# Performance work log

Hardware: AMD Instinct MI355X
Metric: run time of the kernel (lower is better)

The kernel has to match this reference:

```python
import jax, jax.numpy as jnp
import numpy as np
from jax import lax

B, C, L, G = 2048, 9605, 20, 50
ALPHA, ALPHA1, ALPHA2, ALPHA3, ALPHA_OTHER = 0.5, 0.05, 2.0, 10.0, 0.5
NEG_INF = jnp.float32(-1e30)


def setup_inputs() -> dict:
    k0, k1, k2, k3 = jax.random.split(jax.random.key(0), 4)
    x = jax.random.normal(k0, (B, C), jnp.float32)
    # sparse multi-label targets (~10 positives/row) so at most ~1 whitelist group is active,
    # matching the original code's assert len(gt_whitelist_index) == 1
    y = (jax.random.uniform(k1, (B, C)) < 0.001).astype(jnp.int32)
    y_neg = (jax.random.uniform(k2, (B, C)) < 0.001).astype(jnp.int32)
    # L disjoint whitelist groups of G classes each (from mapping_dict in the original)
    idx = jax.random.permutation(k3, C)[: L * G].reshape(L, G)
    group_mask = jnp.zeros((L, C), bool).at[jnp.arange(L)[:, None], idx].set(True)
    return {"x": x, "y": y, "y_neg": y_neg, "group_mask": group_mask}


def _rank_loss(x1, x2, margin):
    # our_rank_loss: sigmoid(alpha3*(x2-x1+margin)), scaled by alpha2 when positive
    d = x2 - x1 + margin
    s = jax.nn.sigmoid(ALPHA3 * d)
    return jnp.where(d > 0, ALPHA2 * s, s)


def reference(x, y, y_neg, group_mask):
    xs = jax.nn.sigmoid(x)  # [B, C]
    gmf = group_mask.astype(jnp.float32)  # [L, C]

    # per-row max score inside each whitelist group -> [B, L]
    # lax.map over the L (=20) groups keeps peak memory at one [B, C] temp per step
    group_max = lax.map(
        lambda m: jnp.max(jnp.where(m, xs, NEG_INF), axis=-1), group_mask
    ).T  # [B, L]

    # find_gt_whitelist: group k active iff sum(y[group_k]) > 0
    active = jnp.einsum("bc,lc->bl", y.astype(jnp.float32), gmf) > 0
    active_neg = jnp.einsum("bc,lc->bl", y_neg.astype(jnp.float32), gmf) > 0
    has_gt = jnp.any(active, axis=-1)  # [B]
    g = jnp.argmax(active, axis=-1)  # first active group (original asserts exactly one)

    # top_k_thres = max(11th largest sigmoid score, alpha_other) in both branches
    thres = jnp.maximum(lax.top_k(xs, 11)[0][:, 10], ALPHA_OTHER)  # [B]

    # max over union of all whitelist classes (wl_indices)
    union_max = jnp.max(jnp.where(jnp.any(group_mask, 0)[None, :], xs, NEG_INF), -1)

    gt_max = jnp.take_along_axis(group_max, g[:, None], axis=1)[:, 0]  # [B]
    # incorrect_max: max(0, max over groups != g); incorrect_neg: max(0, max over neg-active groups)
    excl = jnp.where(jnp.arange(L)[None, :] == g[:, None], NEG_INF, group_max)
    incorrect_max = jnp.maximum(jnp.max(excl, -1), 0.0)
    incorrect_neg = jnp.maximum(jnp.max(jnp.where(active_neg, group_max, 0.0), -1), 0.0)

    # branch A: no gt whitelist group active
    case_a = (1 - ALPHA) * _rank_loss(thres, union_max, ALPHA1) + ALPHA * _rank_loss(
        thres, incorrect_neg, ALPHA1
    )
    # branch B: exactly one gt group g
    case_b = (
        _rank_loss(gt_max, thres, ALPHA1)
        + jnp.where(
            incorrect_max > 0, (1 - ALPHA) * _rank_loss(thres, incorrect_max, ALPHA1), 0.0
        )
        + jnp.where(
            incorrect_neg > 0,
            ALPHA * _rank_loss(thres, incorrect_neg, ALPHA1),
            ALPHA * _rank_loss(thres, incorrect_max, ALPHA1),
        )
    )
    return jnp.sum(jnp.where(has_gt, case_b, case_a))
```

## Files before the change

### kernel.cpp

```cpp
#include <hip/hip_runtime.h>
#include <stdint.h>

#define B_ROWS 2048
#define C_CLS  9605
#define L_GRP  20
#define WAVES  4
#define UNROLL 8

__device__ __forceinline__ float sigmoidf(float v) {
  return 1.0f / (1.0f + __expf(-v));
}

__device__ __forceinline__ float rank_loss(float x1, float x2) {
  float d = x2 - x1 + 0.05f;
  float s = 1.0f / (1.0f + __expf(-10.0f * d));
  return d > 0.0f ? 2.0f * s : s;
}

__device__ __forceinline__ unsigned fmap(float f) {
  unsigned u = __float_as_uint(f);
  return (u & 0x80000000u) ? ~u : (u | 0x80000000u);
}
__device__ __forceinline__ float funmap(unsigned m) {
  unsigned u = (m & 0x80000000u) ? (m ^ 0x80000000u) : ~m;
  return __uint_as_float(u);
}

__global__ void probe_init_kernel(const unsigned char* __restrict__ gm,
                                  unsigned char* __restrict__ gid,
                                  int* __restrict__ cnt) {
  const int tid = blockIdx.x * blockDim.x + threadIdx.x;
  const int nthreads = gridDim.x * blockDim.x;
  for (int i = tid; i < C_CLS; i += nthreads) gid[i] = 0xFF;
  int local = 0;
  for (int i = tid; i < L_GRP * C_CLS; i += nthreads) local += (gm[i] != 0);
#pragma unroll
  for (int off = 32; off; off >>= 1) local += __shfl_xor(local, off);
  if ((threadIdx.x & 63) == 0 && local) atomicAdd(cnt, local);
}

__global__ void build_gid_kernel(const void* gm, const int* __restrict__ cnt,
                                 unsigned char* __restrict__ gid) {
  int i = blockIdx.x * blockDim.x + threadIdx.x;
  if (i >= L_GRP * C_CLS) return;
  const bool is_byte = (*cnt > 600);
  bool m;
  if (is_byte) m = ((const unsigned char*)gm)[i] != 0;
  else         m = ((const unsigned int*)gm)[i] != 0u;
  if (m) {
    int l = i / C_CLS;
    int c = i - l * C_CLS;
    gid[c] = (unsigned char)l;
  }
}

__global__ __launch_bounds__(WAVES * 64) void loss_kernel(
    const float* __restrict__ x, const int* __restrict__ y,
    const int* __restrict__ yn, const unsigned char* __restrict__ gid,
    float* __restrict__ out) {
  __shared__ unsigned s_gmax[WAVES][L_GRP];
  const int lane = threadIdx.x & 63;
  const int wave = threadIdx.x >> 6;
  const int row  = blockIdx.x * WAVES + wave;

  const float* xr = x  + (size_t)row * C_CLS;
  const int*   yr = y  + (size_t)row * C_CLS;
  const int*   nr = yn + (size_t)row * C_CLS;

  if (lane < L_GRP) s_gmax[wave][lane] = 0u;

  float t[11];
#pragma unroll
  for (int i = 0; i < 11; ++i) t[i] = -3.0e38f;
  unsigned actL = 0u, actnL = 0u;

  const int CM = (C_CLS / (64 * UNROLL)) * (64 * UNROLL);
  for (int c = lane; c < CM; c += 64 * UNROLL) {
    float xv[UNROLL]; int yv[UNROLL]; int nv[UNROLL]; unsigned char gv[UNROLL];
#pragma unroll
    for (int k = 0; k < UNROLL; ++k) {
      int cc = c + 64 * k;
      xv[k] = xr[cc]; yv[k] = yr[cc]; nv[k] = nr[cc]; gv[k] = gid[cc];
    }
#pragma unroll
    for (int k = 0; k < UNROLL; ++k) {
      float v = xv[k];
      if (v > t[10]) {
        float a = v;
#pragma unroll
        for (int i = 0; i < 11; ++i) { float hi = fmaxf(t[i], a); a = fminf(t[i], a); t[i] = hi; }
      }
      if (gv[k] < L_GRP) {
        atomicMax(&s_gmax[wave][gv[k]], fmap(v));
        unsigned bit = 1u << gv[k];
        if (yv[k] != 0) actL  |= bit;
        if (nv[k] != 0) actnL |= bit;
      }
    }
  }
  for (int c = CM + lane; c < C_CLS; c += 64) {
    float v = xr[c];
    unsigned char gk = gid[c];
    int yv = yr[c], nv = nr[c];
    if (v > t[10]) {
      float a = v;
#pragma unroll
      for (int i = 0; i < 11; ++i) { float hi = fmaxf(t[i], a); a = fminf(t[i], a); t[i] = hi; }
    }
    if (gk < L_GRP) {
      atomicMax(&s_gmax[wave][gk], fmap(v));
      unsigned bit = 1u << gk;
      if (yv != 0) actL  |= bit;
      if (nv != 0) actnL |= bit;
    }
  }

#pragma unroll
  for (int off = 32; off; off >>= 1) {
    actL  |= __shfl_xor(actL,  off);
    actnL |= __shfl_xor(actnL, off);
  }

  float cur = t[0];
  float eleventh = -3.0e38f;
#pragma unroll
  for (int r = 0; r < 11; ++r) {
    float m = cur;
#pragma unroll
    for (int off = 32; off; off >>= 1) m = fmaxf(m, __shfl_xor(m, off));
    eleventh = m;
    if (r < 10) {
      unsigned long long b = __ballot(cur == m);
      int leader = (int)(__ffsll(b) - 1);
      if (lane == leader) {
#pragma unroll
        for (int i = 0; i < 10; ++i) t[i] = t[i + 1];
        t[10] = -3.0e38f;
        cur = t[0];
      }
    }
  }

  __syncthreads();

  const bool has_gt = (actL != 0u);
  const int g = has_gt ? (__ffs(actL) - 1) : 0;
  const float thres = fmaxf(sigmoidf(eleventh), 0.5f);

  float union_max = -3.0e38f, gt_sg = 0.0f, inc_max = -3.0e38f, inc_neg = 0.0f;
#pragma unroll
  for (int l = 0; l < L_GRP; ++l) {
    float sg = sigmoidf(funmap(s_gmax[wave][l]));
    union_max = fmaxf(union_max, sg);
    if (l == g) gt_sg = sg; else inc_max = fmaxf(inc_max, sg);
    if ((actnL >> l) & 1u) inc_neg = fmaxf(inc_neg, sg);
  }
  inc_max = fmaxf(inc_max, 0.0f);
  inc_neg = fmaxf(inc_neg, 0.0f);

  float loss;
  if (has_gt) {
    loss = rank_loss(gt_sg, thres);
    if (inc_max > 0.0f) loss += 0.5f * rank_loss(thres, inc_max);
    loss += 0.5f * rank_loss(thres, (inc_neg > 0.0f) ? inc_neg : inc_max);
  } else {
    loss = 0.5f * rank_loss(thres, union_max) + 0.5f * rank_loss(thres, inc_neg);
  }
  if (lane == 0) atomicAdd(out, loss);
}

extern "C" void kernel_launch(void* const* d_in, const int* in_sizes, int n_in,
                              void* d_out, int out_size, void* d_ws, size_t ws_size,
                              hipStream_t stream) {
  (void)in_sizes; (void)n_in; (void)ws_size;
  const float* x  = (const float*)d_in[0];
  const int*   y  = (const int*)d_in[1];
  const int*   yn = (const int*)d_in[2];
  const void*  gm = d_in[3];

  int* cnt = (int*)d_ws;
  unsigned char* gid = (unsigned char*)d_ws + 64;

  hipMemsetAsync(d_ws, 0, 64, stream);
  probe_init_kernel<<<188, 256, 0, stream>>>((const unsigned char*)gm, gid, cnt);
  build_gid_kernel<<<(L_GRP * C_CLS + 255) / 256, 256, 0, stream>>>(gm, cnt, gid);

  hipMemsetAsync(d_out, 0, (size_t)out_size * sizeof(float), stream);

  loss_kernel<<<B_ROWS / WAVES, WAVES * 64, 0, stream>>>(x, y, yn, gid,
                                                         (float*)d_out);
}
```

Measured before the change: 264.7 us.

## Assign one block per row with vectorized aligned loads and replicated gid tables

The loss kernel now gives each row a full 256-thread block instead of one wave. Each row is read with float4/int4 loads after peeling to 16-byte alignment, and the gid table is stored as four shifted replicas so that each row's misalignment can use packed 4-byte gid reads. The per-wave top-11 results are merged through shared memory by wave 0, and the group state moves to shared atomics. The two memsets are folded into a single-block probe kernel, which trims launch overhead but serializes the gm scan on one block. The change also adds shared-memory atomics across the four waves and a __syncthreads.

Measured after the change: 252.8 us. -4.5%, faster.

```diff
diff --git a/kernel.cpp b/kernel.cpp
--- a/kernel.cpp
+++ b/kernel.cpp
@@ -4,8 +4,9 @@
 #define B_ROWS 2048
 #define C_CLS  9605
 #define L_GRP  20
-#define WAVES  4
-#define UNROLL 8
+#define GM_BYTES (L_GRP * C_CLS)
+#define REPSTRIDE 9728
+#define NEG_BIG -3.0e38f
 
 __device__ __forceinline__ float sigmoidf(float v) {
   return 1.0f / (1.0f + __expf(-v));
@@ -26,167 +27,214 @@
   return __uint_as_float(u);
 }
 
-__global__ void probe_init_kernel(const unsigned char* __restrict__ gm,
-                                  unsigned char* __restrict__ gid,
-                                  int* __restrict__ cnt) {
-  const int tid = blockIdx.x * blockDim.x + threadIdx.x;
-  const int nthreads = gridDim.x * blockDim.x;
-  for (int i = tid; i < C_CLS; i += nthreads) gid[i] = 0xFF;
+__global__ void probe_init_kernel(const uint4* __restrict__ gm,
+                                  unsigned char* __restrict__ ws,
+                                  float* __restrict__ out,
+                                  int* __restrict__ flag) {
+  __shared__ int s_part[16];
+  const int tid = threadIdx.x;
+  if (tid == 0) out[0] = 0.0f;
+  const int initbytes = 3 * REPSTRIDE + C_CLS + 16;
+  for (int i = tid; i < initbytes; i += 1024) ws[64 + i] = 0xFF;
   int local = 0;
-  for (int i = tid; i < L_GRP * C_CLS; i += nthreads) local += (gm[i] != 0);
+  const int nvec = GM_BYTES / 16;
+  for (int i = tid; i < nvec; i += 1024) {
+    uint4 w = gm[i];
+    unsigned a[4] = {w.x, w.y, w.z, w.w};
+#pragma unroll
+    for (int q = 0; q < 4; ++q) {
+      local += ((a[q] & 0x000000FFu) != 0) + ((a[q] & 0x0000FF00u) != 0) +
+               ((a[q] & 0x00FF0000u) != 0) + ((a[q] & 0xFF000000u) != 0);
+    }
+  }
+  if (tid == 0) {
+    const unsigned char* gb = (const unsigned char*)gm;
+    for (int i = nvec * 16; i < GM_BYTES; ++i) local += (gb[i] != 0);
+  }
 #pragma unroll
   for (int off = 32; off; off >>= 1) local += __shfl_xor(local, off);
-  if ((threadIdx.x & 63) == 0 && local) atomicAdd(cnt, local);
-}
-
-__global__ void build_gid_kernel(const void* gm, const int* __restrict__ cnt,
-                                 unsigned char* __restrict__ gid) {
+  if ((tid & 63) == 0) s_part[tid >> 6] = local;
+  __syncthreads();
+  if (tid == 0) {
+    int tot = 0;
+    for (int w = 0; w < 16; ++w) tot += s_part[w];
+    *flag = tot;
+  }
+}
+
+__global__ void build_gid_kernel(const void* gm, const int* __restrict__ flag,
+                                 unsigned char* __restrict__ ws) {
   int i = blockIdx.x * blockDim.x + threadIdx.x;
-  if (i >= L_GRP * C_CLS) return;
-  const bool is_byte = (*cnt > 600);
+  if (i >= GM_BYTES) return;
+  const bool is_byte = (*flag > 600);
   bool m;
   if (is_byte) m = ((const unsigned char*)gm)[i] != 0;
   else         m = ((const unsigned int*)gm)[i] != 0u;
   if (m) {
     int l = i / C_CLS;
     int c = i - l * C_CLS;
-    gid[c] = (unsigned char)l;
-  }
-}
-
-__global__ __launch_bounds__(WAVES * 64) void loss_kernel(
+    unsigned char* base = ws + 64;
+#pragma unroll
+    for (int r = 0; r < 4; ++r) base[r * REPSTRIDE + r + c] = (unsigned char)l;
+  }
+}
+
+__global__ __launch_bounds__(256, 4) void loss_kernel(
     const float* __restrict__ x, const int* __restrict__ y,
-    const int* __restrict__ yn, const unsigned char* __restrict__ gid,
+    const int* __restrict__ yn, const unsigned char* __restrict__ ws64,
     float* __restrict__ out) {
-  __shared__ unsigned s_gmax[WAVES][L_GRP];
-  const int lane = threadIdx.x & 63;
-  const int wave = threadIdx.x >> 6;
-  const int row  = blockIdx.x * WAVES + wave;
-
-  const float* xr = x  + (size_t)row * C_CLS;
-  const int*   yr = y  + (size_t)row * C_CLS;
-  const int*   nr = yn + (size_t)row * C_CLS;
-
-  if (lane < L_GRP) s_gmax[wave][lane] = 0u;
+  __shared__ unsigned s_gmax[L_GRP];
+  __shared__ unsigned s_act, s_actn;
+  __shared__ float s_wtop[4 * 11];
+  const int tid = threadIdx.x;
+  const int lane = tid & 63;
+  const int wave = tid >> 6;
+  const int row = blockIdx.x;
+
+  const size_t base = (size_t)row * C_CLS;
+  const int mis = (int)(base & 3);
+  const int peel = (4 - mis) & 3;
+  const float* xr = x + base;
+  const int* yr = y + base;
+  const int* nr = yn + base;
+  const unsigned char* gidc = ws64 + mis * REPSTRIDE + mis;
+
+  if (tid < L_GRP) s_gmax[tid] = 0u;
+  if (tid == 0) { s_act = 0u; s_actn = 0u; }
+  __syncthreads();
 
   float t[11];
 #pragma unroll
-  for (int i = 0; i < 11; ++i) t[i] = -3.0e38f;
+  for (int i = 0; i < 11; ++i) t[i] = NEG_BIG;
   unsigned actL = 0u, actnL = 0u;
 
-  const int CM = (C_CLS / (64 * UNROLL)) * (64 * UNROLL);
-  for (int c = lane; c < CM; c += 64 * UNROLL) {
-    float xv[UNROLL]; int yv[UNROLL]; int nv[UNROLL]; unsigned char gv[UNROLL];
-#pragma unroll
-    for (int k = 0; k < UNROLL; ++k) {
-      int cc = c + 64 * k;
-      xv[k] = xr[cc]; yv[k] = yr[cc]; nv[k] = nr[cc]; gv[k] = gid[cc];
-    }
-#pragma unroll
-    for (int k = 0; k < UNROLL; ++k) {
-      float v = xv[k];
-      if (v > t[10]) {
-        float a = v;
-#pragma unroll
-        for (int i = 0; i < 11; ++i) { float hi = fmaxf(t[i], a); a = fminf(t[i], a); t[i] = hi; }
-      }
-      if (gv[k] < L_GRP) {
-        atomicMax(&s_gmax[wave][gv[k]], fmap(v));
-        unsigned bit = 1u << gv[k];
-        if (yv[k] != 0) actL  |= bit;
-        if (nv[k] != 0) actnL |= bit;
-      }
-    }
-  }
-  for (int c = CM + lane; c < C_CLS; c += 64) {
-    float v = xr[c];
-    unsigned char gk = gid[c];
-    int yv = yr[c], nv = nr[c];
+  auto process = [&](float v, unsigned gk, int yv, int nv) {
     if (v > t[10]) {
       float a = v;
 #pragma unroll
-      for (int i = 0; i < 11; ++i) { float hi = fmaxf(t[i], a); a = fminf(t[i], a); t[i] = hi; }
+      for (int i = 0; i < 11; ++i) {
+        float hi = fmaxf(t[i], a); a = fminf(t[i], a); t[i] = hi;
+      }
     }
     if (gk < L_GRP) {
-      atomicMax(&s_gmax[wave][gk], fmap(v));
+      atomicMax(&s_gmax[gk], fmap(v));
       unsigned bit = 1u << gk;
-      if (yv != 0) actL  |= bit;
+      if (yv != 0) actL |= bit;
       if (nv != 0) actnL |= bit;
     }
-  }
-
-#pragma unroll
-  for (int off = 32; off; off >>= 1) {
-    actL  |= __shfl_xor(actL,  off);
-    actnL |= __shfl_xor(actnL, off);
-  }
+  };
+
+  if (tid < peel) process(xr[tid], gidc[tid], yr[tid], nr[tid]);
+
+  const int nvec = (C_CLS - peel) >> 2;
+  const float4* x4 = (const float4*)(xr + peel);
+  const int4* y4 = (const int4*)(yr + peel);
+  const int4* n4 = (const int4*)(nr + peel);
+  const unsigned* g4 = (const unsigned*)(gidc + peel);
+  for (int j = tid; j < nvec; j += 256) {
+    float4 xv = x4[j];
+    int4 yv = y4[j];
+    int4 nv = n4[j];
+    unsigned gw = g4[j];
+    process(xv.x, gw & 0xFFu, yv.x, nv.x);
+    process(xv.y, (gw >> 8) & 0xFFu, yv.y, nv.y);
+    process(xv.z, (gw >> 16) & 0xFFu, yv.z, nv.z);
+    process(xv.w, gw >> 24, yv.w, nv.w);
+  }
+  const int tail0 = peel + (nvec << 2);
+  const int rem = C_CLS - tail0;
+  if (tid < rem) {
+    int c = tail0 + tid;
+    process(xr[c], gidc[c], yr[c], nr[c]);
+  }
+
+  if (actL) atomicOr(&s_act, actL);
+  if (actnL) atomicOr(&s_actn, actnL);
 
   float cur = t[0];
-  float eleventh = -3.0e38f;
+  float mr[11];
 #pragma unroll
   for (int r = 0; r < 11; ++r) {
     float m = cur;
 #pragma unroll
     for (int off = 32; off; off >>= 1) m = fmaxf(m, __shfl_xor(m, off));
-    eleventh = m;
+    mr[r] = m;
     if (r < 10) {
       unsigned long long b = __ballot(cur == m);
       int leader = (int)(__ffsll(b) - 1);
       if (lane == leader) {
 #pragma unroll
         for (int i = 0; i < 10; ++i) t[i] = t[i + 1];
-        t[10] = -3.0e38f;
+        t[10] = NEG_BIG;
         cur = t[0];
       }
     }
   }
-
+  if (lane == 0) {
+#pragma unroll
+    for (int r = 0; r < 11; ++r) s_wtop[wave * 11 + r] = mr[r];
+  }
   __syncthreads();
 
-  const bool has_gt = (actL != 0u);
-  const int g = has_gt ? (__ffs(actL) - 1) : 0;
-  const float thres = fmaxf(sigmoidf(eleventh), 0.5f);
-
-  float union_max = -3.0e38f, gt_sg = 0.0f, inc_max = -3.0e38f, inc_neg = 0.0f;
-#pragma unroll
-  for (int l = 0; l < L_GRP; ++l) {
-    float sg = sigmoidf(funmap(s_gmax[wave][l]));
-    union_max = fmaxf(union_max, sg);
-    if (l == g) gt_sg = sg; else inc_max = fmaxf(inc_max, sg);
-    if ((actnL >> l) & 1u) inc_neg = fmaxf(inc_neg, sg);
-  }
-  inc_max = fmaxf(inc_max, 0.0f);
-  inc_neg = fmaxf(inc_neg, 0.0f);
-
-  float loss;
-  if (has_gt) {
-    loss = rank_loss(gt_sg, thres);
-    if (inc_max > 0.0f) loss += 0.5f * rank_loss(thres, inc_max);
-    loss += 0.5f * rank_loss(thres, (inc_neg > 0.0f) ? inc_neg : inc_max);
-  } else {
-    loss = 0.5f * rank_loss(thres, union_max) + 0.5f * rank_loss(thres, inc_neg);
-  }
-  if (lane == 0) atomicAdd(out, loss);
+  if (wave == 0) {
+    float v = (lane < 44) ? s_wtop[lane] : NEG_BIG;
+    float eleventh = NEG_BIG;
+#pragma unroll
+    for (int r = 0; r < 11; ++r) {
+      float m = v;
+#pragma unroll
+      for (int off = 32; off; off >>= 1) m = fmaxf(m, __shfl_xor(m, off));
+      eleventh = m;
+      if (r < 10) {
+        unsigned long long b = __ballot(v == m);
+        int leader = (int)(__ffsll(b) - 1);
+        if (lane == leader) v = NEG_BIG;
+      }
+    }
+
+    const unsigned aL = s_act, anL = s_actn;
+    const bool has_gt = (aL != 0u);
+    const int g = has_gt ? (__ffs(aL) - 1) : 0;
+    const float thres = fmaxf(sigmoidf(eleventh), 0.5f);
+
+    float union_max = NEG_BIG, gt_sg = 0.0f, inc_max = NEG_BIG, inc_neg = 0.0f;
+#pragma unroll
+    for (int l = 0; l < L_GRP; ++l) {
+      float sg = sigmoidf(funmap(s_gmax[l]));
+      union_max = fmaxf(union_max, sg);
+      if (l == g) gt_sg = sg; else inc_max = fmaxf(inc_max, sg);
+      if ((anL >> l) & 1u) inc_neg = fmaxf(inc_neg, sg);
+    }
+    inc_max = fmaxf(inc_max, 0.0f);
+    inc_neg = fmaxf(inc_neg, 0.0f);
+
+    float loss;
+    if (has_gt) {
+      loss = rank_loss(gt_sg, thres);
+      if (inc_max > 0.0f) loss += 0.5f * rank_loss(thres, inc_max);
+      loss += 0.5f * rank_loss(thres, (inc_neg > 0.0f) ? inc_neg : inc_max);
+    } else {
+      loss = 0.5f * rank_loss(thres, union_max) + 0.5f * rank_loss(thres, inc_neg);
+    }
+    if (lane == 0) atomicAdd(out, loss);
+  }
 }
 
 extern "C" void kernel_launch(void* const* d_in, const int* in_sizes, int n_in,
                               void* d_out, int out_size, void* d_ws, size_t ws_size,
                               hipStream_t stream) {
-  (void)in_sizes; (void)n_in; (void)ws_size;
-  const float* x  = (const float*)d_in[0];
-  const int*   y  = (const int*)d_in[1];
-  const int*   yn = (const int*)d_in[2];
-  const void*  gm = d_in[3];
-
-  int* cnt = (int*)d_ws;
-  unsigned char* gid = (unsigned char*)d_ws + 64;
-
-  hipMemsetAsync(d_ws, 0, 64, stream);
-  probe_init_kernel<<<188, 256, 0, stream>>>((const unsigned char*)gm, gid, cnt);
-  build_gid_kernel<<<(L_GRP * C_CLS + 255) / 256, 256, 0, stream>>>(gm, cnt, gid);
-
-  hipMemsetAsync(d_out, 0, (size_t)out_size * sizeof(float), stream);
-
-  loss_kernel<<<B_ROWS / WAVES, WAVES * 64, 0, stream>>>(x, y, yn, gid,
-                                                         (float*)d_out);
-}
+  (void)in_sizes; (void)n_in; (void)out_size; (void)ws_size;
+  const float* x = (const float*)d_in[0];
+  const int* y = (const int*)d_in[1];
+  const int* yn = (const int*)d_in[2];
+  const void* gm = d_in[3];
+
+  int* flag = (int*)d_ws;
+  unsigned char* ws = (unsigned char*)d_ws;
+  unsigned char* ws64 = ws + 64;
+
+  probe_init_kernel<<<1, 1024, 0, stream>>>((const uint4*)gm, ws,
+                                            (float*)d_out, flag);
+  build_gid_kernel<<<(GM_BYTES + 255) / 256, 256, 0, stream>>>(gm, flag, ws);
+  loss_kernel<<<B_ROWS, 256, 0, stream>>>(x, y, yn, ws64, (float*)d_out);
+}
```
